# Optimization experiments

Measured on AMD Instinct MI355X. Metric: run time of the kernel, lower is better.

Reference implementation:

```python
import jax, jax.numpy as jnp
import numpy as np

BIG = 1e9  # finite stand-in for float('inf') border padding (grad-safe)


def setup_inputs() -> dict:
    key = jax.random.key(0)
    k1, k2 = jax.random.split(key)
    B, L1, L2, F = 32, 1024, 1024, 128
    return {
        "seq1": jax.random.normal(k1, (B, L1, F), dtype=jnp.float32),
        "seq2": jax.random.normal(k2, (B, L2, F), dtype=jnp.float32),
        "scale_weights": jnp.ones((1,), dtype=jnp.float32),  # nn.Parameter ones(num_scales)/num_scales -> softmax-normalized anyway
    }


def _dtw_similarity(seq1, seq2):
    """Vectorized (anti-diagonal wavefront) version of MultiScaleDTW._compute_dtw.

    Same recurrence: D[i,j] = ||s1[i-1]-s2[j-1]|| + min(D[i-1,j-1], D[i-1,j], D[i,j-1]),
    D[0,0]=0, first row/col = inf. Returns similarity = 1/(1 + D[L1,L2]/(L1+L2)).
    """
    B, L1, F = seq1.shape
    L2 = seq2.shape[1]
    # pairwise L2 distance matrix (B, L1, L2) via |a|^2 + |b|^2 - 2 a.b (one GEMM)
    sq1 = jnp.sum(seq1 * seq1, axis=-1)
    sq2 = jnp.sum(seq2 * seq2, axis=-1)
    dot = jnp.einsum('bif,bjf->bij', seq1, seq2)
    C = jnp.sqrt(jnp.maximum(sq1[:, :, None] + sq2[:, None, :] - 2.0 * dot, 0.0))

    i_idx = jnp.arange(L1 + 1)
    # diagonal k holds D[i, k-i] for i in [0, L1]
    d0 = jnp.full((B, L1 + 1), BIG, jnp.float32).at[:, 0].set(0.0)  # k=0: D[0,0]=0
    d1 = jnp.full((B, L1 + 1), BIG, jnp.float32)                     # k=1: borders = inf

    def shift(x):  # x[:, i] -> x[:, i-1], pad with BIG
        return jnp.concatenate([jnp.full((B, 1), BIG, x.dtype), x[:, :-1]], axis=1)

    def step(carry, k):
        prev2, prev = carry  # diagonals k-2, k-1
        j = k - i_idx
        row = jnp.clip(i_idx - 1, 0, L1 - 1)
        col = jnp.clip(j - 1, 0, L2 - 1)
        c = C[:, row, col]  # (B, L1+1) cost along the diagonal
        m = jnp.minimum(shift(prev2), jnp.minimum(shift(prev), prev))
        cur = c + m
        valid = (i_idx >= 1) & (i_idx <= L1) & (j >= 1) & (j <= L2)
        cur = jnp.where(valid[None, :], cur, BIG)
        return (prev, cur), None

    (_, last), _ = jax.lax.scan(step, (d0, d1), jnp.arange(2, L1 + L2 + 1))
    dtw_dist = last[:, L1] / (L1 + L2)  # D[L1, L2] / (L1 + L2)
    return 1.0 / (1.0 + dtw_dist)


def reference(seq1, seq2, scale_weights):
    # num_scales = 1: softmax over single scale weight -> 1.0; only scale-0 DTW runs
    w = jax.nn.softmax(scale_weights, axis=0)
    sim = _dtw_similarity(seq1, seq2)
    return w[0] * sim  # combined_similarity, shape (B,)
```

## Files before the change

### kernel.cpp

```cpp
#include <hip/hip_runtime.h>
#include <hip/hip_bf16.h>

#define BIGV 1.0e9f

static constexpr int B_ = 32;
static constexpr int L_ = 1024;
static constexpr int F_ = 128;
static constexpr int S_ = 2;
static constexpr int UDIM_ = 1296;
static constexpr int LAG_ = 160;
static constexpr int NSEGL_ = 72;
static constexpr int NSEGG_ = 82;
static constexpr size_t STREAM_US = (size_t)B_ * 2 * UDIM_ * 512;

typedef __attribute__((ext_vector_type(8))) short short8;
typedef __attribute__((ext_vector_type(4))) float f32x4;

__device__ __forceinline__ unsigned pack2(float x, float y) {
  unsigned r;
  asm("v_cvt_pk_bf16_f32 %0, %1, %2" : "=v"(r) : "v"(x), "v"(y));
  return r;
}

__global__ void norm_kernel(const float* __restrict__ s1, const float* __restrict__ s2,
                            float* __restrict__ nrm) {
  int gt   = blockIdx.x * blockDim.x + threadIdx.x;
  int wid  = gt >> 6;
  int lane = gt & 63;
  const float* src = (wid < B_ * L_) ? (s1 + (size_t)wid * F_)
                                     : (s2 + (size_t)(wid - B_ * L_) * F_);
  float2 v = ((const float2*)src)[lane];
  float s = v.x * v.x + v.y * v.y;
#pragma unroll
  for (int o = 32; o > 0; o >>= 1) s += __shfl_xor(s, o, 64);
  if (lane == 0) nrm[wid] = s;
}

__global__ __launch_bounds__(256) void cost_kernel(const float* __restrict__ s1,
                                                   const float* __restrict__ s2,
                                                   ushort* __restrict__ stream,
                                                   const float* __restrict__ nrm) {
  __shared__ __align__(16) ushort sbuf[2 * 128 * 136];
  __shared__ float q1[128], q2[128];
  short (*aL)[136] = (short(*)[136])sbuf;
  short (*bL)[136] = (short(*)[136])(sbuf + 128 * 136);
  ushort (*stage)[136] = (ushort(*)[136])sbuf;

  const int tid = threadIdx.x;
  const int b   = blockIdx.y;
  const int tc  = blockIdx.x & 7;
  const int tr  = blockIdx.x >> 3;

  const float* Ap = s1 + (size_t)b * L_ * F_ + (size_t)tr * 128 * F_;
  const float* Bp = s2 + (size_t)b * L_ * F_ + (size_t)tc * 128 * F_;

#pragma unroll 4
  for (int it = 0; it < 16; ++it) {
    int idx = it * 1024 + tid * 4;
    int r = idx >> 7, cc = idx & 127;
    float4 va = *(const float4*)(Ap + idx);
    float4 vb = *(const float4*)(Bp + idx);
    *(uint2*)&aL[r][cc] = make_uint2(pack2(va.x, va.y), pack2(va.z, va.w));
    *(uint2*)&bL[r][cc] = make_uint2(pack2(vb.x, vb.y), pack2(vb.z, vb.w));
  }
  if (tid < 128) q1[tid] = nrm[(size_t)b * L_ + tr * 128 + tid];
  else           q2[tid - 128] = nrm[(size_t)B_ * L_ + (size_t)b * L_ + tc * 128 + (tid - 128)];
  __syncthreads();

  const int wave = tid >> 6, lane = tid & 63, quad = lane >> 4, l16 = lane & 15;
  const int m0 = (wave >> 1) * 64, n0 = (wave & 1) * 64;

  f32x4 acc[4][4] = {};
#pragma unroll
  for (int kc = 0; kc < 4; ++kc) {
    short8 af[4], bf[4];
#pragma unroll
    for (int mi = 0; mi < 4; ++mi)
      af[mi] = *(const short8*)&aL[m0 + mi * 16 + l16][kc * 32 + quad * 8];
#pragma unroll
    for (int nj = 0; nj < 4; ++nj)
      bf[nj] = *(const short8*)&bL[n0 + nj * 16 + l16][kc * 32 + quad * 8];
#pragma unroll
    for (int mi = 0; mi < 4; ++mi)
#pragma unroll
      for (int nj = 0; nj < 4; ++nj)
        acc[mi][nj] = __builtin_amdgcn_mfma_f32_16x16x32_bf16(af[mi], bf[nj], acc[mi][nj], 0, 0, 0);
  }

  __syncthreads();

#pragma unroll
  for (int mi = 0; mi < 4; ++mi) {
    int lr = m0 + mi * 16 + quad * 4;
    int du = 2 * (lr >> 3);
    float a0 = q1[lr + 0], a1 = q1[lr + 1], a2 = q1[lr + 2], a3 = q1[lr + 3];
#pragma unroll
    for (int nj = 0; nj < 4; ++nj) {
      int lc = n0 + nj * 16 + l16;
      float qc = q2[lc];
      float vx = sqrtf(fmaxf(a0 + qc - 2.0f * acc[mi][nj][0], 0.0f));
      float vy = sqrtf(fmaxf(a1 + qc - 2.0f * acc[mi][nj][1], 0.0f));
      float vz = sqrtf(fmaxf(a2 + qc - 2.0f * acc[mi][nj][2], 0.0f));
      float vw = sqrtf(fmaxf(a3 + qc - 2.0f * acc[mi][nj][3], 0.0f));
      *(uint2*)&stage[lc + du][lr] = make_uint2(pack2(vx, vy), pack2(vz, vw));
    }
  }
  __syncthreads();

  const int w      = tr >> 2;
  const int rlbase = (tr & 3) * 128;
  const int ubase  = tc * 128 + 32 * (tr & 3);
  ushort* Sb = stream + ((size_t)(b * 2 + w) * UDIM_ + ubase) * 512 + rlbase;
#pragma unroll
  for (int it = 0; it < 10; ++it) {
    int t = it * 256 + tid;
    if (t < 158 * 16) {
      int u = t >> 4, g = t & 15;
      if ((unsigned)(u - 2 * g) < 128u)
        *(uint4*)(Sb + (size_t)u * 512 + g * 8) = *(const uint4*)&stage[u][g * 8];
    }
  }
}

#define UNPACK_CV(cw, cv)                         \
  cv[0] = __uint_as_float((cw).x << 16);          \
  cv[1] = __uint_as_float((cw).x & 0xFFFF0000u);  \
  cv[2] = __uint_as_float((cw).y << 16);          \
  cv[3] = __uint_as_float((cw).y & 0xFFFF0000u);  \
  cv[4] = __uint_as_float((cw).z << 16);          \
  cv[5] = __uint_as_float((cw).z & 0xFFFF0000u);  \
  cv[6] = __uint_as_float((cw).w << 16);          \
  cv[7] = __uint_as_float((cw).w & 0xFFFF0000u);

#define CHAIN_BODY(head)                                            \
  {                                                                 \
    float cur = (head);                                             \
    float nl[8];                                                    \
    nl[0] = cur;                                                    \
    _Pragma("unroll") for (int r = 1; r < 8; ++r) {                 \
      cur = cv[r] + fminf(fminf(left[r - 1], left[r]), cur);        \
      nl[r] = cur;                                                  \
    }                                                               \
    _Pragma("unroll") for (int r = 0; r < 8; ++r) left[r] = nl[r];  \
    bot = nl[7];                                                    \
  }

__global__ __launch_bounds__(256, 1) void dtw_kernel(const ushort* __restrict__ stream,
                                                     float* __restrict__ out) {
  __shared__ ushort ldsA[2][16][512];
  __shared__ ushort ldsB[2][16][512];
  __shared__ float hand[1040];

  const int b    = blockIdx.x;
  const int tid  = threadIdx.x;
  const int wave = tid >> 6;
  const int lane = tid & 63;

  if (wave >= 2) {
    const int ls = wave - 2;
    const ushort* src = stream + (size_t)(b * 2 + ls) * UDIM_ * 512;
    auto loadSeg = [&](int g, int buf) {
      ushort(*dst)[512] = ls ? ldsB[buf] : ldsA[buf];
#pragma unroll
      for (int i = 0; i < 16; ++i) {
        const uint4* sp = (const uint4*)(src + (size_t)(g * 16 + i) * 512);
        *(uint4*)&dst[i][lane * 8] = sp[lane];
      }
    };
    if (ls == 0) loadSeg(0, 0);
    for (int n = 0; n < NSEGG_; ++n) {
      __syncthreads();
      int g = (ls == 0) ? (n + 1) : (n - 9);
      if ((unsigned)g < (unsigned)NSEGL_) loadSeg(g, g & 1);
    }
    return;
  }

  const bool l0 = (lane == 0);
  float left[8];
#pragma unroll
  for (int r = 0; r < 8; ++r) left[r] = BIGV;
  float bot = BIGV;
  float sh[4] = {BIGV, BIGV, BIGV, BIGV};
  float hPrev = BIGV, result = 0.0f;
  float hRing[4];
  float hb[16];
  uint4 pre[4];

  for (int n = 0; n < NSEGG_; ++n) {
    __syncthreads();
    const int sBase = 16 * n - (wave ? LAG_ : 0);
    if ((unsigned)sBase >= 1152u) continue;

    const ushort(*lds)[512] = wave ? ldsB[(sBase >> 4) & 1] : ldsA[(sBase >> 4) & 1];
#pragma unroll
    for (int i = 0; i < 4; ++i) pre[i] = *(const uint4*)&lds[i][lane * 8];

    const bool fast = (sBase >= 128) & (sBase <= 1008);

    if (wave == 0) {
      if (fast) {
#pragma unroll
        for (int k = 0; k < 16; ++k) {
          float shN = __shfl_up(bot, 1, 64);
          uint4 cw = pre[k & 3];
          if (k < 12) pre[k & 3] = *(const uint4*)&lds[k + 4][lane * 8];
          float cv[8];
          UNPACK_CV(cw, cv)
          float dgT = l0 ? BIGV : sh[(k + 2) & 3];
          float upT = l0 ? BIGV : sh[(k + 3) & 3];
          CHAIN_BODY(cv[0] + fminf(fminf(dgT, upT), left[0]))
          sh[k & 3] = shN;
          hb[k] = bot;
        }
        if (lane == 63) {
          float4* hp = (float4*)&hand[sBase - 126];
          hp[0] = make_float4(hb[0], hb[1], hb[2], hb[3]);
          hp[1] = make_float4(hb[4], hb[5], hb[6], hb[7]);
          hp[2] = make_float4(hb[8], hb[9], hb[10], hb[11]);
          hp[3] = make_float4(hb[12], hb[13], hb[14], hb[15]);
        }
      } else {
#pragma unroll
        for (int k = 0; k < 16; ++k) {
          const int s = sBase + k;
          const int col = s - S_ * lane;
          float shN = __shfl_up(bot, 1, 64);
          uint4 cw = pre[k & 3];
          if (k < 12) pre[k & 3] = *(const uint4*)&lds[k + 4][lane * 8];
          float cv[8];
          UNPACK_CV(cw, cv)
          float dgT = l0 ? ((s == 0) ? 0.0f : BIGV) : sh[(k + 2) & 3];
          float upT = l0 ? BIGV : sh[(k + 3) & 3];
          bool act = ((unsigned)col < 1024u);
          float c0 = act ? cv[0] : BIGV;
          CHAIN_BODY(c0 + fminf(fminf(dgT, upT), left[0]))
          sh[k & 3] = shN;
          int j = s - 126;
          if (lane == 63 && (unsigned)j < 1024u) hand[j] = bot;
        }
      }
    } else {
      if (fast) {
#pragma unroll
        for (int i = 0; i < 4; ++i) hRing[i] = hand[sBase + i];
#pragma unroll
        for (int k = 0; k < 16; ++k) {
          float shN = __shfl_up(bot, 1, 64);
          float hCur = hRing[k & 3];
          uint4 cw = pre[k & 3];
          if (k < 12) pre[k & 3] = *(const uint4*)&lds[k + 4][lane * 8];
          hRing[k & 3] = hand[sBase + k + 4];
          float cv[8];
          UNPACK_CV(cw, cv)
          float dgT = l0 ? hPrev : sh[(k + 2) & 3];
          float upT = l0 ? hCur : sh[(k + 3) & 3];
          CHAIN_BODY(cv[0] + fminf(fminf(dgT, upT), left[0]))
          sh[k & 3] = shN;
          hPrev = hCur;
        }
      } else {
#pragma unroll
        for (int i = 0; i < 4; ++i) hRing[i] = hand[(sBase + i) & 1023];
#pragma unroll
        for (int k = 0; k < 16; ++k) {
          const int s = sBase + k;
          const int col = s - S_ * lane;
          float shN = __shfl_up(bot, 1, 64);
          float hCur = hRing[k & 3];
          uint4 cw = pre[k & 3];
          if (k < 12) pre[k & 3] = *(const uint4*)&lds[k + 4][lane * 8];
          hRing[k & 3] = hand[(s + 4) & 1023];
          float cv[8];
          UNPACK_CV(cw, cv)
          float dgT = l0 ? ((s == 0) ? BIGV : hPrev) : sh[(k + 2) & 3];
          float upT = l0 ? hCur : sh[(k + 3) & 3];
          bool act = ((unsigned)col < 1024u);
          float c0 = act ? cv[0] : BIGV;
          CHAIN_BODY(c0 + fminf(fminf(dgT, upT), left[0]))
          sh[k & 3] = shN;
          hPrev = hCur;
          if (s == 1149) result = bot;
        }
      }
    }
  }
  if (wave == 1 && lane == 63) out[b] = 1.0f / (1.0f + result * (1.0f / 2048.0f));
}

extern "C" void kernel_launch(void* const* d_in, const int* in_sizes, int n_in,
                              void* d_out, int out_size, void* d_ws, size_t ws_size,
                              hipStream_t stream_) {
  const float* s1 = (const float*)d_in[0];
  const float* s2 = (const float*)d_in[1];
  float* out = (float*)d_out;
  ushort* cws = (ushort*)d_ws;
  float* nrm = (float*)(cws + STREAM_US);

  norm_kernel<<<dim3((2 * B_ * L_) / 4), 256, 0, stream_>>>(s1, s2, nrm);
  cost_kernel<<<dim3(64, B_), 256, 0, stream_>>>(s1, s2, cws, nrm);
  dtw_kernel<<<dim3(B_), 256, 0, stream_>>>(cws, out);
}
```

Measured before the change: 223.6 us.

## Replace LDS producer waves with direct global register prefetch in DTW kernel

Removes the two loader waves and the LDS double buffers. The two compute waves now prefetch cost rows straight from global memory into a 16-entry register ring, 16 steps ahead. This cuts the LDS staging traffic and the producer overhead, and halves the block size. In exchange, the serial recurrence is exposed to global/L2 latency with a limited prefetch distance, and register pressure rises.

```diff
diff --git a/kernel.cpp b/kernel.cpp
--- a/kernel.cpp
+++ b/kernel.cpp
@@ -9,7 +9,6 @@
 static constexpr int S_ = 2;
 static constexpr int UDIM_ = 1296;
 static constexpr int LAG_ = 160;
-static constexpr int NSEGL_ = 72;
 static constexpr int NSEGG_ = 82;
 static constexpr size_t STREAM_US = (size_t)B_ * 2 * UDIM_ * 512;
 
@@ -145,38 +144,18 @@
     bot = nl[7];                                                    \
   }
 
-__global__ __launch_bounds__(256, 1) void dtw_kernel(const ushort* __restrict__ stream,
+__global__ __launch_bounds__(128, 1) void dtw_kernel(const ushort* __restrict__ stream,
                                                      float* __restrict__ out) {
-  __shared__ ushort ldsA[2][16][512];
-  __shared__ ushort ldsB[2][16][512];
   __shared__ float hand[1040];
 
   const int b    = blockIdx.x;
   const int tid  = threadIdx.x;
   const int wave = tid >> 6;
   const int lane = tid & 63;
-
-  if (wave >= 2) {
-    const int ls = wave - 2;
-    const ushort* src = stream + (size_t)(b * 2 + ls) * UDIM_ * 512;
-    auto loadSeg = [&](int g, int buf) {
-      ushort(*dst)[512] = ls ? ldsB[buf] : ldsA[buf];
-#pragma unroll
-      for (int i = 0; i < 16; ++i) {
-        const uint4* sp = (const uint4*)(src + (size_t)(g * 16 + i) * 512);
-        *(uint4*)&dst[i][lane * 8] = sp[lane];
-      }
-    };
-    if (ls == 0) loadSeg(0, 0);
-    for (int n = 0; n < NSEGG_; ++n) {
-      __syncthreads();
-      int g = (ls == 0) ? (n + 1) : (n - 9);
-      if ((unsigned)g < (unsigned)NSEGL_) loadSeg(g, g & 1);
-    }
-    return;
-  }
-
   const bool l0 = (lane == 0);
+
+  const ushort* src = stream + (size_t)(b * 2 + wave) * UDIM_ * 512 + lane * 8;
+
   float left[8];
 #pragma unroll
   for (int r = 0; r < 8; ++r) left[r] = BIGV;
@@ -185,17 +164,16 @@
   float hPrev = BIGV, result = 0.0f;
   float hRing[4];
   float hb[16];
-  uint4 pre[4];
+  uint4 pre[16];
+
+#pragma unroll
+  for (int i = 0; i < 16; ++i) pre[i] = *(const uint4*)(src + (size_t)i * 512);
 
   for (int n = 0; n < NSEGG_; ++n) {
     __syncthreads();
     const int sBase = 16 * n - (wave ? LAG_ : 0);
     if ((unsigned)sBase >= 1152u) continue;
 
-    const ushort(*lds)[512] = wave ? ldsB[(sBase >> 4) & 1] : ldsA[(sBase >> 4) & 1];
-#pragma unroll
-    for (int i = 0; i < 4; ++i) pre[i] = *(const uint4*)&lds[i][lane * 8];
-
     const bool fast = (sBase >= 128) & (sBase <= 1008);
 
     if (wave == 0) {
@@ -203,8 +181,8 @@
 #pragma unroll
         for (int k = 0; k < 16; ++k) {
           float shN = __shfl_up(bot, 1, 64);
-          uint4 cw = pre[k & 3];
-          if (k < 12) pre[k & 3] = *(const uint4*)&lds[k + 4][lane * 8];
+          uint4 cw = pre[k];
+          pre[k] = *(const uint4*)(src + (size_t)(sBase + k + 16) * 512);
           float cv[8];
           UNPACK_CV(cw, cv)
           float dgT = l0 ? BIGV : sh[(k + 2) & 3];
@@ -226,8 +204,8 @@
           const int s = sBase + k;
           const int col = s - S_ * lane;
           float shN = __shfl_up(bot, 1, 64);
-          uint4 cw = pre[k & 3];
-          if (k < 12) pre[k & 3] = *(const uint4*)&lds[k + 4][lane * 8];
+          uint4 cw = pre[k];
+          pre[k] = *(const uint4*)(src + (size_t)(sBase + k + 16) * 512);
           float cv[8];
           UNPACK_CV(cw, cv)
           float dgT = l0 ? ((s == 0) ? 0.0f : BIGV) : sh[(k + 2) & 3];
@@ -248,8 +226,8 @@
         for (int k = 0; k < 16; ++k) {
           float shN = __shfl_up(bot, 1, 64);
           float hCur = hRing[k & 3];
-          uint4 cw = pre[k & 3];
-          if (k < 12) pre[k & 3] = *(const uint4*)&lds[k + 4][lane * 8];
+          uint4 cw = pre[k];
+          pre[k] = *(const uint4*)(src + (size_t)(sBase + k + 16) * 512);
           hRing[k & 3] = hand[sBase + k + 4];
           float cv[8];
           UNPACK_CV(cw, cv)
@@ -268,8 +246,8 @@
           const int col = s - S_ * lane;
           float shN = __shfl_up(bot, 1, 64);
           float hCur = hRing[k & 3];
-          uint4 cw = pre[k & 3];
-          if (k < 12) pre[k & 3] = *(const uint4*)&lds[k + 4][lane * 8];
+          uint4 cw = pre[k];
+          pre[k] = *(const uint4*)(src + (size_t)(sBase + k + 16) * 512);
           hRing[k & 3] = hand[(s + 4) & 1023];
           float cv[8];
           UNPACK_CV(cw, cv)
@@ -299,5 +277,5 @@
 
   norm_kernel<<<dim3((2 * B_ * L_) / 4), 256, 0, stream_>>>(s1, s2, nrm);
   cost_kernel<<<dim3(64, B_), 256, 0, stream_>>>(s1, s2, cws, nrm);
-  dtw_kernel<<<dim3(B_), 256, 0, stream_>>>(cws, out);
-}
+  dtw_kernel<<<dim3(B_), 128, 0, stream_>>>(cws, out);
+}
```

Result: slower. 237.6 us (+6.3%).
